# Kernel tuning notes

Hardware: AMD Instinct MI355X
Metric: run time of the kernel (lower is better)

Reference implementation:

```python
import jax, jax.numpy as jnp
import numpy as np

NCA_HIDDEN = 16
N_CODES = 32
EMBED_DIM = 64


def conv2d(x, w, pad, b=None):
    # x: (N, Cin, H, W), w: (Cout, Cin, kh, kw)
    y = jax.lax.conv_general_dilated(
        x, w, window_strides=(1, 1), padding=[(pad, pad), (pad, pad)],
        dimension_numbers=('NCHW', 'OIHW', 'NCHW'))
    if b is not None:
        y = y + b[None, :, None, None]
    return y


def setup_inputs() -> dict:
    key = jax.random.key(0)
    ks = jax.random.split(key, 32)
    rn = lambda k, shp, s=0.05: jax.random.normal(k, shp, dtype=jnp.float32) * s
    H = NCA_HIDDEN
    upd = H * H * 3 * 3  # 2304
    tau = H * H          # 256
    inp = {
        'demo_inputs':  jax.random.normal(ks[0], (8, 1, 64, 64), dtype=jnp.float32),
        'demo_outputs': jax.random.normal(ks[1], (8, 1, 64, 64), dtype=jnp.float32),
        'test_input':   jax.random.normal(ks[2], (16, 1, 256, 256), dtype=jnp.float32),
        # TaskEncoder params
        'enc_w1': rn(ks[3], (16, 2, 3, 3)),  'enc_b1': jnp.zeros((16,), jnp.float32),
        'enc_w2': rn(ks[4], (32, 16, 3, 3)), 'enc_b2': jnp.zeros((32,), jnp.float32),
        'enc_lw': rn(ks[5], (EMBED_DIM, 32)), 'enc_lb': jnp.zeros((EMBED_DIM,), jnp.float32),
        # gen_update hypernet
        'gu_w1': rn(ks[6], (128, EMBED_DIM)), 'gu_b1': jnp.zeros((128,), jnp.float32),
        'gu_w2': rn(ks[7], (upd, 128)),       'gu_b2': jnp.zeros((upd,), jnp.float32),
        # gen_tau hypernet
        'gt_w1': rn(ks[8], (64, EMBED_DIM)),  'gt_b1': jnp.zeros((64,), jnp.float32),
        'gt_w2': rn(ks[9], (tau, 64)),        'gt_b2': jnp.zeros((tau,), jnp.float32),
        # stem
        'stem_w': rn(ks[10], (H, 1, 3, 3)), 'stem_b': jnp.zeros((H,), jnp.float32),
        # VQ codebook, init U(-1/n_codes, 1/n_codes)
        'codebook': jax.random.uniform(ks[11], (N_CODES, H), jnp.float32,
                                       minval=-1.0 / N_CODES, maxval=1.0 / N_CODES),
        # decoder 1x1 conv
        'dec_w': rn(ks[12], (1, H, 1, 1)), 'dec_b': jnp.zeros((1,), jnp.float32),
        'n_steps': 5,
    }
    return inp


def reference(demo_inputs, demo_outputs, test_input,
              enc_w1, enc_b1, enc_w2, enc_b2, enc_lw, enc_lb,
              gu_w1, gu_b1, gu_w2, gu_b2,
              gt_w1, gt_b1, gt_w2, gt_b2,
              stem_w, stem_b, codebook, dec_w, dec_b, n_steps):
    H = NCA_HIDDEN
    # --- Task encoder: mean task embedding over demo pairs ---
    pairs = jnp.concatenate([demo_inputs, demo_outputs], axis=1)  # (N,2,h,w)
    h = jax.nn.relu(conv2d(pairs, enc_w1, 1, enc_b1))
    h = jax.nn.relu(conv2d(h, enc_w2, 1, enc_b2))
    h = h.mean(axis=(2, 3))                   # AdaptiveAvgPool2d(1)+Flatten -> (N,32)
    te = (h @ enc_lw.T + enc_lb).mean(axis=0)  # (embed_dim,)
    # --- Hypernetworks generate NCA weights ---
    W_update = (jax.nn.relu(te @ gu_w1.T + gu_b1) @ gu_w2.T + gu_b2).reshape(H, H, 3, 3)
    W_tau = (jax.nn.relu(te @ gt_w1.T + gt_b1) @ gt_w2.T + gt_b2).reshape(H, H, 1, 1)
    # --- Stem ---
    state = jax.nn.relu(conv2d(test_input, stem_w, 1, stem_b))  # (B,16,Hh,Ww)
    cb_sq = (codebook ** 2).sum(axis=1)  # (n_codes,)
    for _ in range(int(n_steps)):
        delta = jax.nn.relu(conv2d(state, W_update, 1))
        beta = jax.nn.sigmoid(conv2d(state, W_tau, 0))
        state = beta * state + (1.0 - beta) * delta
        # --- VQ step (straight-through) ---
        B, C, Hh, Ww = state.shape
        zf = state.transpose(0, 2, 3, 1).reshape(-1, C)  # (B*Hh*Ww, C)
        dists = (zf ** 2).sum(1, keepdims=True) + cb_sq - 2.0 * (zf @ codebook.T)
        idx = jnp.argmin(dists, axis=1)
        zq = codebook[idx].reshape(B, Hh, Ww, C).transpose(0, 3, 1, 2)
        state = state + jax.lax.stop_gradient(zq - state)
    output = jax.nn.sigmoid(conv2d(state, dec_w, 0, dec_b))
    return output
```

## Files before the change

### kernel.cpp

```cpp
#include <hip/hip_runtime.h>
#include <stdint.h>

#define NPIX 65536
#define NIMG 16

typedef float4 F4;
typedef _Float16 h2v __attribute__((ext_vector_type(2)));
typedef _Float16 h8v __attribute__((ext_vector_type(8)));
typedef float    f4v __attribute__((ext_vector_type(4)));

union H8 { h8v v; h2v p[4]; _Float16 e[8]; };

__device__ __forceinline__ float sigm(float x){ return 1.0f/(1.0f+__expf(-x)); }

#if defined(__has_builtin)
#if __has_builtin(__builtin_amdgcn_rcpf)
#define FRCP(x) __builtin_amdgcn_rcpf(x)
#endif
#endif
#ifndef FRCP
#define FRCP(x) (1.0f/(x))
#endif
__device__ __forceinline__ float sigmf(float x){ return FRCP(1.0f + __expf(-x)); }

__device__ __forceinline__ h2v pkrtz(float a, float b){
  return __builtin_bit_cast(h2v, __builtin_amdgcn_cvt_pkrtz(a,b));
}

#if defined(__has_builtin)
#if __has_builtin(__builtin_amdgcn_fdot2)
#define FDOT2(a,b,c) __builtin_amdgcn_fdot2((a),(b),(c),false)
#endif
#endif
#ifndef FDOT2
#define FDOT2(a,b,c) ((c) + (float)(a)[0]*(float)(b)[0] + (float)(a)[1]*(float)(b)[1])
#endif

__global__ __launch_bounds__(256) void k_prep(
    const float* __restrict__ w2, _Float16* __restrict__ wfragE)
{
  int t=threadIdx.x;
  for(int i=t;i<5120;i+=256){
    int j=i&7, rest=i>>3, lane=rest&63, rest2=rest>>6, ks=rest2%5, b=rest2/5;
    int g=lane>>4, nn=lane&15;
    int k=32*ks+8*g+j;
    float v=0.f;
    if(k<144){
      int tap=2*ks+(g>>1), ci=8*(g&1)+j, co=b*16+nn;
      v=w2[co*144+ci*9+tap];
    }
    wfragE[i]=(_Float16)v;
  }
}

__global__ __launch_bounds__(256) void k_enc(
    const float* __restrict__ din, const float* __restrict__ dou,
    const float* __restrict__ w1, const float* __restrict__ b1,
    const float* __restrict__ b2,
    const _Float16* __restrict__ wfragE,
    float* __restrict__ pooled)
{
  __shared__ float2 in_s[400];
  __shared__ h8v st_h[324*3];
  __shared__ float red[4][32];
  __shared__ h2v stwp_s[144];
  __shared__ h2v stbp_s[8];

  const int tid=threadIdx.x;
  const int bx=blockIdx.x, by=blockIdx.y, n=blockIdx.z;
  const float* i0 = din + n*4096;
  const float* i1 = dou + n*4096;

  for(int i=tid;i<400;i+=256){
    int sy=i/20, sx=i-sy*20;
    int gy=by*16-2+sy, gx=bx*16-2+sx;
    bool ok=((unsigned)gy<64u && (unsigned)gx<64u);
    in_s[i] = ok ? make_float2(i0[gy*64+gx], i1[gy*64+gx]) : make_float2(0.f,0.f);
  }
  if(tid<144){
    int q=tid/18, r=tid-18*q;
    stwp_s[tid]=pkrtz(w1[36*q+r], w1[36*q+18+r]);
  } else if(tid<152){
    int q=tid-144;
    stbp_s[q]=pkrtz(b1[2*q], b1[2*q+1]);
  }

  const int lane=tid&63, w=tid>>6, g=lane>>4, nn=lane&15;
  h8v B0[5], B1[5];
  const h8v* wfE=(const h8v*)wfragE;
  #pragma unroll
  for(int ks=0;ks<5;ks++){ B0[ks]=wfE[ks*64+lane]; B1[ks]=wfE[(5+ks)*64+lane]; }
  float b2a=b2[nn], b2b=b2[nn+16];
  __syncthreads();

  for(int p=tid;p<324;p+=256){
    int syh=p/18, sxh=p-syh*18;
    int gy=by*16-1+syh, gx=bx*16-1+sxh;
    H8 o0,o1;
    if((unsigned)gy<64u && (unsigned)gx<64u){
      h2v a2[8];
      #pragma unroll
      for(int q=0;q<8;q++) a2[q]=stbp_s[q];
      #pragma unroll
      for(int ky=0;ky<3;ky++){
        #pragma unroll
        for(int kx=0;kx<3;kx++){
          int tp=ky*3+kx;
          float2 v=in_s[(syh+ky)*20+(sxh+kx)];
          h2v v0=pkrtz(v.x,v.x), v1=pkrtz(v.y,v.y);
          #pragma unroll
          for(int q=0;q<8;q++){
            a2[q]=stwp_s[(2*q)*9+tp]*v0 + a2[q];
            a2[q]=stwp_s[(2*q+1)*9+tp]*v1 + a2[q];
          }
        }
      }
      o0.p[0]=a2[0]; o0.p[1]=a2[1]; o0.p[2]=a2[2]; o0.p[3]=a2[3];
      o1.p[0]=a2[4]; o1.p[1]=a2[5]; o1.p[2]=a2[6]; o1.p[3]=a2[7];
      #pragma unroll
      for(int c=0;c<8;c++){
        o0.e[c]=o0.e[c]>(_Float16)0?o0.e[c]:(_Float16)0;
        o1.e[c]=o1.e[c]>(_Float16)0?o1.e[c]:(_Float16)0;
      }
    } else {
      o0.v=(h8v){0,0,0,0,0,0,0,0};
      o1.v=(h8v){0,0,0,0,0,0,0,0};
    }
    st_h[p*3]  =o0.v;
    st_h[p*3+1]=o1.v;
  }
  __syncthreads();

  f4v acc0[4], acc1[4];
  #pragma unroll
  for(int m=0;m<4;m++){ acc0[m]=(f4v){0.f,0.f,0.f,0.f}; acc1[m]=(f4v){0.f,0.f,0.f,0.f}; }
  #pragma unroll
  for(int ks=0;ks<5;ks++){
    int t=2*ks+(g>>1); if(t>8) t=8;
    int tyo=(t*11)>>5, txo=t-tyo*3;
    int sel=g&1;
    #pragma unroll
    for(int m=0;m<4;m++){
      int sy=4*w+m+tyo;
      h8v a=st_h[(sy*18+nn+txo)*3+sel];
      acc0[m]=__builtin_amdgcn_mfma_f32_16x16x32_f16(a,B0[ks],acc0[m],0,0,0);
      acc1[m]=__builtin_amdgcn_mfma_f32_16x16x32_f16(a,B1[ks],acc1[m],0,0,0);
    }
  }
  float s0=0.f, s1=0.f;
  #pragma unroll
  for(int m=0;m<4;m++)
    #pragma unroll
    for(int r=0;r<4;r++){
      s0+=fmaxf(acc0[m][r]+b2a,0.f);
      s1+=fmaxf(acc1[m][r]+b2b,0.f);
    }
  s0+=__shfl_down(s0,32,64); s0+=__shfl_down(s0,16,64);
  s1+=__shfl_down(s1,32,64); s1+=__shfl_down(s1,16,64);
  if(lane<16){ red[w][nn]=s0; red[w][nn+16]=s1; }
  __syncthreads();
  if(tid<32){
    float s=red[0][tid]+red[1][tid]+red[2][tid]+red[3][tid];
    atomicAdd(&pooled[n*32+tid], s);
  }
}

__global__ __launch_bounds__(256) void k_hyperA(
    const float* __restrict__ pooled,
    const float* __restrict__ lw, const float* __restrict__ lb,
    const float* __restrict__ guw1, const float* __restrict__ gub1,
    const float* __restrict__ gtw1, const float* __restrict__ gtb1,
    const float* __restrict__ gtw2, const float* __restrict__ gtb2,
    const float* __restrict__ cb, const float* __restrict__ decw, const float* __restrict__ decb,
    float* __restrict__ hid_g,
    _Float16* __restrict__ wfrag_g,
    _Float16* __restrict__ Mh_g,
    _Float16* __restrict__ bcb_g, _Float16* __restrict__ omb_g,
    _Float16* __restrict__ cbh_g,
    float* __restrict__ chs_g, float* __restrict__ dvals_g)
{
  __shared__ float hm[32], te_s[64], hid_s[128], hidt_s[64];
  __shared__ float wt_s[256];
  __shared__ float cb_s[512];
  int t = threadIdx.x;
  for(int i=t;i<2560;i+=256) ((unsigned int*)wfrag_g)[i]=0u;
  for(int i=t;i<2508;i+=256) ((unsigned int*)Mh_g)[i]=0u;
  if(t<32){
    float s=0.f;
    for(int n=0;n<8;n++) s += pooled[n*32+t];
    hm[t] = s * (1.0f/32768.0f);
  }
  for(int i=t;i<512;i+=256) cb_s[i]=cb[i];
  __syncthreads();
  if(t<64){
    float s=lb[t];
    for(int c=0;c<32;c++) s = fmaf(lw[t*32+c], hm[c], s);
    te_s[t]=s;
  }
  __syncthreads();
  if(t<128){
    float s=gub1[t];
    for(int j=0;j<64;j++) s = fmaf(guw1[t*64+j], te_s[j], s);
    s=fmaxf(s,0.f);
    hid_s[t]=s; hid_g[t]=s;
  } else if(t<192){
    int i=t-128;
    float s=gtb1[i];
    for(int j=0;j<64;j++) s = fmaf(gtw1[i*64+j], te_s[j], s);
    hidt_s[i]=fmaxf(s,0.f);
  }
  __syncthreads();
  {
    float s=gtb2[t];
    for(int i=0;i<64;i++) s = fmaf(gtw2[t*64+i], hidt_s[i], s);
    int co=t>>4, ci=t&15;
    wt_s[ci*16+co]=s;
  }
  __syncthreads();
  {
    int ci=t>>4, co=t&15;
    int g=ci>>3, j=ci&7, lane=(g<<4)|co;
    wfrag_g[(448+lane)*8+j]=(_Float16)wt_s[ci*16+co];
  }
  for(int o=t;o<512;o+=256){
    int k=o>>4, c=o&15;
    float T=0.f;
    for(int ci=0;ci<16;ci++) T = fmaf(wt_s[ci*16+c], cb_s[k*16+ci], T);
    float beta=sigm(T);
    bcb_g[o]=(_Float16)(beta*cb_s[o]);
    omb_g[o]=(_Float16)(1.f-beta);
    cbh_g[o]=(_Float16)cb_s[o];
  }
  if(t<32){
    float sq=0.f, d=0.f;
    for(int c=0;c<16;c++){ float v=cb_s[t*16+c]; sq=fmaf(v,v,sq); d=fmaf(decw[c],v,d); }
    chs_g[t]=0.5f*sq;
    dvals_g[t]=sigm(d+decb[0]);
  }
}

__global__ __launch_bounds__(256) void k_hyperB(
    const float* __restrict__ guw2, const float* __restrict__ gub2,
    const float* __restrict__ hid_g, const float* __restrict__ cb,
    _Float16* __restrict__ wfrag_g, _Float16* __restrict__ Mh_g)
{
  __shared__ float hid_s[128];
  __shared__ float wu_s[256];
  __shared__ float cb_s[512];
  const int t=threadIdx.x, tp=blockIdx.x;
  if(t<128) hid_s[t]=hid_g[t];
  for(int i=t;i<512;i+=256) cb_s[i]=cb[i];
  __syncthreads();
  const int ci=t>>4, co=t&15;
  const int o=co*144+ci*9+tp;
  float s=gub2[o];
  const F4* gp=(const F4*)(guw2+(size_t)o*128);
  #pragma unroll
  for(int i=0;i<32;i++){
    F4 g=gp[i];
    s=fmaf(g.x,hid_s[4*i],s); s=fmaf(g.y,hid_s[4*i+1],s);
    s=fmaf(g.z,hid_s[4*i+2],s); s=fmaf(g.w,hid_s[4*i+3],s);
  }
  wu_s[ci*16+co]=s;
  {
    int k=tp*16+ci;
    int ks=k>>5, rem=k&31, g2=rem>>3, j=rem&7, lane=(g2<<4)|co;
    wfrag_g[(ks*64+lane)*8+j]=(_Float16)s;
  }
  __syncthreads();
  for(int o2=t;o2<512;o2+=256){
    int k=o2>>4, c=o2&15;
    float m=0.f;
    for(int c2=0;c2<16;c2++) m=fmaf(wu_s[c2*16+c], cb_s[k*16+c2], m);
    Mh_g[k*152+tp*16+c]=(_Float16)m;
  }
}

#define ST_STRIDE 3
struct S1P1 { h8v st[324*ST_STRIDE]; float in[400]; };
union S1U { S1P1 p; unsigned int dt[256*20]; };

__global__ __launch_bounds__(256) void k_step1(
    const float* __restrict__ tin,
    const float* __restrict__ stw, const float* __restrict__ stb,
    const _Float16* __restrict__ wfrag,
    const _Float16* __restrict__ cbh, const float* __restrict__ chs,
    uint8_t* __restrict__ idx_out)
{
  __shared__ S1U u;
  __shared__ h8v cb8_s[64];
  __shared__ float chs_s[32];
  __shared__ h2v stwp_s[72];
  __shared__ h2v stbp_s[8];

  const int tid=threadIdx.x;
  const int bx=blockIdx.x, by=blockIdx.y, n=blockIdx.z;
  const float* in = tin + (size_t)n*NPIX;

  for(int i=tid;i<400;i+=256){
    int sy=i/20, sx=i-sy*20;
    int gy=by*16-2+sy, gx=bx*16-2+sx;
    u.p.in[i] = ((unsigned)gy<256u && (unsigned)gx<256u) ? in[gy*256+gx] : 0.0f;
  }
  if(tid<72){
    int q=tid/9, tp=tid-q*9;
    stwp_s[q*9+tp]=pkrtz(stw[(2*q)*9+tp], stw[(2*q+1)*9+tp]);
  } else if(tid<80){
    int q=tid-72;
    stbp_s[q]=pkrtz(stb[2*q], stb[2*q+1]);
  } else if(tid>=160 && tid<192) chs_s[tid-160]=chs[tid-160];
  if(tid<64) ((uint4*)cb8_s)[tid] = ((const uint4*)cbh)[tid];

  const int lane = tid & 63, w = tid >> 6;
  const int g = lane >> 4, nn = lane & 15;
  h8v Bd[5], Bt2;
  const h8v* wf = (const h8v*)wfrag;
  #pragma unroll
  for(int ks=0;ks<5;ks++) Bd[ks]=wf[ks*64+lane];
  Bt2 = wf[7*64+lane];

  __syncthreads();

  for(int p=tid;p<324;p+=256){
    int syh=p/18, sxh=p-syh*18;
    int gy=by*16-1+syh, gx=bx*16-1+sxh;
    H8 b0,b1;
    if((unsigned)gy<256u && (unsigned)gx<256u){
      h2v a2[8];
      #pragma unroll
      for(int q=0;q<8;q++) a2[q]=stbp_s[q];
      #pragma unroll
      for(int ky=0;ky<3;ky++){
        #pragma unroll
        for(int kx=0;kx<3;kx++){
          int tp=ky*3+kx;
          float v=u.p.in[(syh+ky)*20+(sxh+kx)];
          h2v vv=pkrtz(v,v);
          #pragma unroll
          for(int q=0;q<8;q++) a2[q] = stwp_s[q*9+tp]*vv + a2[q];
        }
      }
      b0.p[0]=a2[0]; b0.p[1]=a2[1]; b0.p[2]=a2[2]; b0.p[3]=a2[3];
      b1.p[0]=a2[4]; b1.p[1]=a2[5]; b1.p[2]=a2[6]; b1.p[3]=a2[7];
      #pragma unroll
      for(int c=0;c<8;c++){
        b0.e[c]=b0.e[c]>(_Float16)0?b0.e[c]:(_Float16)0;
        b1.e[c]=b1.e[c]>(_Float16)0?b1.e[c]:(_Float16)0;
      }
    } else {
      b0.v=(h8v){0,0,0,0,0,0,0,0};
      b1.v=(h8v){0,0,0,0,0,0,0,0};
    }
    u.p.st[p*ST_STRIDE]  =b0.v;
    u.p.st[p*ST_STRIDE+1]=b1.v;
  }
  __syncthreads();

  f4v accd[4], acct[4];
  #pragma unroll
  for(int m=0;m<4;m++){ accd[m]=(f4v){0.f,0.f,0.f,0.f}; acct[m]=(f4v){0.f,0.f,0.f,0.f}; }
  #pragma unroll
  for(int ks=0;ks<5;ks++){
    int t = 2*ks + (g>>1); if(t>8) t=8;
    int tyo=(t*11)>>5, txo=t-tyo*3;
    int sel = g&1;
    #pragma unroll
    for(int m=0;m<4;m++){
      int sy = 4*w+m+tyo;
      h8v a = u.p.st[(sy*18 + nn + txo)*ST_STRIDE + sel];
      accd[m]=__builtin_amdgcn_mfma_f32_16x16x32_f16(a,Bd[ks],accd[m],0,0,0);
      if(ks==2) acct[m]=__builtin_amdgcn_mfma_f32_16x16x32_f16(a,Bt2,acct[m],0,0,0);
    }
  }
  const int py=tid>>4, pxx=tid&15;
  const int cpx=((py+1)*18+pxx+1)*ST_STRIDE;
  h8v z0=u.p.st[cpx], z1=u.p.st[cpx+1];
  __syncthreads();

  #pragma unroll
  for(int m=0;m<4;m++){
    #pragma unroll
    for(int r=0;r<4;r++){
      int px=(4*w+m)*16 + g*4 + r;
      h2v pk = pkrtz(accd[m][r], acct[m][r]);
      u.dt[px*20+nn] = __builtin_bit_cast(unsigned int, pk);
    }
  }
  __syncthreads();

  const uint4* dr=(const uint4*)(u.dt+tid*20);
  uint4 q0=dr[0],q1=dr[1],q2=dr[2],q3=dr[3];
  unsigned int qq[16]={q0.x,q0.y,q0.z,q0.w,q1.x,q1.y,q1.z,q1.w,
                       q2.x,q2.y,q2.z,q2.w,q3.x,q3.y,q3.z,q3.w};
  float zn[16];
  #pragma unroll
  for(int c=0;c<16;c++){
    h2v dt2=__builtin_bit_cast(h2v, qq[c]);
    float d=(float)dt2[0]; d = d>0.f?d:0.f;
    float beta=sigmf((float)dt2[1]);
    float zv = (c<8)? (float)z0[c] : (float)z1[c-8];
    zn[c]=fmaf(beta, zv-d, d);
  }
  H8 u0,u1;
  #pragma unroll
  for(int j=0;j<4;j++){
    u0.p[j]=pkrtz(zn[2*j],zn[2*j+1]);
    u1.p[j]=pkrtz(zn[8+2*j],zn[9+2*j]);
  }
  int best=0; float bv=-3.4e38f;
  #pragma unroll
  for(int k=0;k<32;k++){
    H8 c0,c1; c0.v=cb8_s[k*2]; c1.v=cb8_s[k*2+1];
    float dot=0.f;
    #pragma unroll
    for(int j=0;j<4;j++) dot=FDOT2(u0.p[j],c0.p[j],dot);
    #pragma unroll
    for(int j=0;j<4;j++) dot=FDOT2(u1.p[j],c1.p[j],dot);
    float val=dot-chs_s[k];
    if(val>bv){bv=val;best=k;}
  }
  idx_out[(size_t)n*NPIX + (by*16+py)*256 + (bx*16+pxx)]=(uint8_t)best;
}

__global__ __launch_bounds__(256) void k_stepN(
    const uint8_t* __restrict__ idx_in,
    const uint4* __restrict__ Mh,
    const _Float16* __restrict__ bcbh, const _Float16* __restrict__ ombh,
    const _Float16* __restrict__ cbh,  const float* __restrict__ chs,
    const float* __restrict__ dvals,
    uint8_t* __restrict__ idx_out, float* __restrict__ out, int last)
{
  __shared__ int id_s[324];
  __shared__ uint4 M_s[627];
  __shared__ h8v bcb_s[64], omb_s[64], cb8_s[64];
  __shared__ float chs_s[32], dv_s[32];
  const int tid=threadIdx.x;
  const int bx=blockIdx.x, by=blockIdx.y, n=blockIdx.z;
  const uint8_t* ip = idx_in + (size_t)n*NPIX;

  for(int i=tid;i<324;i+=256){
    int sy=i/18, sx=i-sy*18;
    int gy=by*16-1+sy, gx=bx*16-1+sx;
    id_s[i] = ((unsigned)gy<256u && (unsigned)gx<256u) ? (int)ip[gy*256+gx] : 32;
  }
  for(int i=tid;i<627;i+=256) M_s[i]=Mh[i];
  if(tid<64)        ((uint4*)bcb_s)[tid]     = ((const uint4*)bcbh)[tid];
  else if(tid<128)  ((uint4*)omb_s)[tid-64]  = ((const uint4*)ombh)[tid-64];
  else if(tid<192)  ((uint4*)cb8_s)[tid-128] = ((const uint4*)cbh)[tid-128];
  else if(tid<224)  chs_s[tid-192]=chs[tid-192];
  else              dv_s[tid-224]=dvals[tid-224];
  __syncthreads();

  const int py=tid>>4, pxx=tid&15;
  int ida[9];
  #pragma unroll
  for(int dy=0;dy<3;dy++)
    #pragma unroll
    for(int dx=0;dx<3;dx++)
      ida[dy*3+dx]=id_s[(py+dy)*18+pxx+dx];

  const h8v* Mv=(const h8v*)M_s;
  h8v a0={0,0,0,0,0,0,0,0}, a1={0,0,0,0,0,0,0,0};
  #pragma unroll
  for(int t=0;t<9;t++){
    const h8v* mp=&Mv[ida[t]*19+t*2];
    a0+=mp[0]; a1+=mp[1];
  }
  int kc=ida[4];
  h8v r0,r1;
  #pragma unroll
  for(int q=0;q<8;q++){
    r0[q]=a0[q]>(_Float16)0?a0[q]:(_Float16)0;
    r1[q]=a1[q]>(_Float16)0?a1[q]:(_Float16)0;
  }
  H8 u0,u1;
  u0.v = bcb_s[kc*2]   + omb_s[kc*2]  *r0;
  u1.v = bcb_s[kc*2+1] + omb_s[kc*2+1]*r1;
  int best=0; float bv=-3.4e38f;
  #pragma unroll
  for(int k=0;k<32;k++){
    H8 c0,c1; c0.v=cb8_s[k*2]; c1.v=cb8_s[k*2+1];
    float dot=0.f;
    #pragma unroll
    for(int j=0;j<4;j++) dot=FDOT2(u0.p[j],c0.p[j],dot);
    #pragma unroll
    for(int j=0;j<4;j++) dot=FDOT2(u1.p[j],c1.p[j],dot);
    float val=dot-chs_s[k];
    if(val>bv){bv=val;best=k;}
  }
  size_t gidx=(size_t)n*NPIX + (size_t)(by*16+py)*256 + bx*16+pxx;
  if(last) out[gidx]=dv_s[best];
  else     idx_out[gidx]=(uint8_t)best;
}

extern "C" void kernel_launch(void* const* d_in, const int* in_sizes, int n_in,
                              void* d_out, int out_size, void* d_ws, size_t ws_size,
                              hipStream_t stream)
{
  const float* demo_in  = (const float*)d_in[0];
  const float* demo_out = (const float*)d_in[1];
  const float* test_in  = (const float*)d_in[2];
  const float* enc_w1 = (const float*)d_in[3];
  const float* enc_b1 = (const float*)d_in[4];
  const float* enc_w2 = (const float*)d_in[5];
  const float* enc_b2 = (const float*)d_in[6];
  const float* enc_lw = (const float*)d_in[7];
  const float* enc_lb = (const float*)d_in[8];
  const float* gu_w1 = (const float*)d_in[9];
  const float* gu_b1 = (const float*)d_in[10];
  const float* gu_w2 = (const float*)d_in[11];
  const float* gu_b2 = (const float*)d_in[12];
  const float* gt_w1 = (const float*)d_in[13];
  const float* gt_b1 = (const float*)d_in[14];
  const float* gt_w2 = (const float*)d_in[15];
  const float* gt_b2 = (const float*)d_in[16];
  const float* stem_w = (const float*)d_in[17];
  const float* stem_b = (const float*)d_in[18];
  const float* codebook = (const float*)d_in[19];
  const float* dec_w = (const float*)d_in[20];
  const float* dec_b = (const float*)d_in[21];

  float* ws = (float*)d_ws;
  float* pooled = ws;
  float* chs    = pooled + 256;
  float* dvals  = chs + 32;
  float* hid_g  = dvals + 32;
  _Float16* hbase = (_Float16*)(ws + 448);
  _Float16* wfrag  = hbase;
  _Float16* wfragE = hbase + 5120;
  _Float16* Mh     = hbase + 10240;
  _Float16* bcbh   = hbase + 15264;
  _Float16* ombh   = hbase + 15776;
  _Float16* cbh    = hbase + 16288;
  uint8_t* idxA = (uint8_t*)(hbase + 16800);
  uint8_t* idxB = idxA + (size_t)NIMG*NPIX;

  (void)hipMemsetAsync(pooled, 0, 256*sizeof(float), stream);
  k_prep<<<1,256,0,stream>>>(enc_w2, wfragE);
  k_enc<<<dim3(4,4,8),256,0,stream>>>(demo_in, demo_out, enc_w1, enc_b1, enc_b2, wfragE, pooled);
  k_hyperA<<<1,256,0,stream>>>(pooled, enc_lw, enc_lb,
                               gu_w1,gu_b1, gt_w1,gt_b1, gt_w2,gt_b2,
                               codebook, dec_w, dec_b,
                               hid_g, wfrag, Mh, bcbh, ombh, cbh, chs, dvals);
  k_hyperB<<<9,256,0,stream>>>(gu_w2, gu_b2, hid_g, codebook, wfrag, Mh);
  dim3 tgrid(16,16,NIMG);
  k_step1<<<tgrid,256,0,stream>>>(test_in, stem_w, stem_b, wfrag, cbh, chs, idxA);
  float* outp = (float*)d_out;
  k_stepN<<<tgrid,256,0,stream>>>(idxA,(const uint4*)Mh,bcbh,ombh,cbh,chs,dvals, idxB,outp,0);
  k_stepN<<<tgrid,256,0,stream>>>(idxB,(const uint4*)Mh,bcbh,ombh,cbh,chs,dvals, idxA,outp,0);
  k_stepN<<<tgrid,256,0,stream>>>(idxA,(const uint4*)Mh,bcbh,ombh,cbh,chs,dvals, idxB,outp,0);
  k_stepN<<<tgrid,256,0,stream>>>(idxB,(const uint4*)Mh,bcbh,ombh,cbh,chs,dvals, idxA,outp,1);
}
```

Measured before the change: 250.3 us.

## Compute VQ codebook distances with MFMA and cross-lane argmin

Replaces the per-thread 32-code FDOT2 distance loop in both step kernels with a 16x16x32 f16 MFMA. Each pixel's quantized state is staged in LDS and multiplied against a pre-swizzled codebook fragment built in the hypernet kernel. The argmin is then taken with xor shuffles within each 16-lane group. This moves the scalar dot-product work onto matrix cores, at the cost of an extra LDS round trip, shuffle reductions, a wave barrier, and half of the MFMA K dimension padded with zeros.

```diff
diff --git a/kernel.cpp b/kernel.cpp
--- a/kernel.cpp
+++ b/kernel.cpp
@@ -27,14 +27,37 @@
   return __builtin_bit_cast(h2v, __builtin_amdgcn_cvt_pkrtz(a,b));
 }
 
-#if defined(__has_builtin)
-#if __has_builtin(__builtin_amdgcn_fdot2)
-#define FDOT2(a,b,c) __builtin_amdgcn_fdot2((a),(b),(c),false)
-#endif
-#endif
-#ifndef FDOT2
-#define FDOT2(a,b,c) ((c) + (float)(a)[0]*(float)(b)[0] + (float)(a)[1]*(float)(b)[1])
-#endif
+__device__ __forceinline__ int vq_mfma(
+    const _Float16* zn_s, uint8_t* bs,
+    h8v B0, h8v B1, float ch0, float ch1, int tid)
+{
+  const int lane=tid&63, wv=tid>>6, g=lane>>4, nn=lane&15;
+  __builtin_amdgcn_wave_barrier();
+  #pragma unroll
+  for(int g2=0;g2<4;g2++){
+    f4v D0={0.f,0.f,0.f,0.f}, D1={0.f,0.f,0.f,0.f};
+    h8v a=(h8v){0,0,0,0,0,0,0,0};
+    if(g<2) a=*(const h8v*)(zn_s + (wv*64+g2*16+nn)*24 + g*8);
+    D0=__builtin_amdgcn_mfma_f32_16x16x32_f16(a,B0,D0,0,0,0);
+    D1=__builtin_amdgcn_mfma_f32_16x16x32_f16(a,B1,D1,0,0,0);
+    #pragma unroll
+    for(int r=0;r<4;r++){
+      float v0=D0[r]-ch0, v1=D1[r]-ch1;
+      bool t1=v1>v0;
+      float val=t1?v1:v0; int idx=t1?nn+16:nn;
+      #pragma unroll
+      for(int mm=1;mm<16;mm<<=1){
+        float vo=__shfl_xor(val,mm,64);
+        int io=__shfl_xor(idx,mm,64);
+        bool tk=(vo>val)||((vo==val)&&(io<idx));
+        val=tk?vo:val; idx=tk?io:idx;
+      }
+      if(nn==4*g+r) bs[wv*64+g2*16+4*g+r]=(uint8_t)idx;
+    }
+  }
+  __builtin_amdgcn_wave_barrier();
+  return (int)bs[tid];
+}
 
 __global__ __launch_bounds__(256) void k_prep(
     const float* __restrict__ w2, _Float16* __restrict__ wfragE)
@@ -176,7 +199,7 @@
     _Float16* __restrict__ wfrag_g,
     _Float16* __restrict__ Mh_g,
     _Float16* __restrict__ bcb_g, _Float16* __restrict__ omb_g,
-    _Float16* __restrict__ cbh_g,
+    _Float16* __restrict__ vqb_g,
     float* __restrict__ chs_g, float* __restrict__ dvals_g)
 {
   __shared__ float hm[32], te_s[64], hid_s[128], hidt_s[64];
@@ -222,6 +245,12 @@
     int g=ci>>3, j=ci&7, lane=(g<<4)|co;
     wfrag_g[(448+lane)*8+j]=(_Float16)wt_s[ci*16+co];
   }
+  for(int i=t;i<1024;i+=256){
+    int j=i&7, lane=(i>>3)&63, b=i>>9;
+    int g=lane>>4, nn=lane&15, k=g*8+j;
+    float v=(k<16)? cb_s[(b*16+nn)*16+k] : 0.f;
+    vqb_g[i]=(_Float16)v;
+  }
   for(int o=t;o<512;o+=256){
     int k=o>>4, c=o&15;
     float T=0.f;
@@ -229,7 +258,6 @@
     float beta=sigm(T);
     bcb_g[o]=(_Float16)(beta*cb_s[o]);
     omb_g[o]=(_Float16)(1.f-beta);
-    cbh_g[o]=(_Float16)cb_s[o];
   }
   if(t<32){
     float sq=0.f, d=0.f;
@@ -278,18 +306,17 @@
 
 #define ST_STRIDE 3
 struct S1P1 { h8v st[324*ST_STRIDE]; float in[400]; };
-union S1U { S1P1 p; unsigned int dt[256*20]; };
+struct S1VQ { alignas(16) _Float16 zn[256*24]; uint8_t bs[256]; };
+union S1U { S1P1 p; unsigned int dt[256*20]; S1VQ v; };
 
 __global__ __launch_bounds__(256) void k_step1(
     const float* __restrict__ tin,
     const float* __restrict__ stw, const float* __restrict__ stb,
     const _Float16* __restrict__ wfrag,
-    const _Float16* __restrict__ cbh, const float* __restrict__ chs,
+    const _Float16* __restrict__ vqb, const float* __restrict__ chs,
     uint8_t* __restrict__ idx_out)
 {
   __shared__ S1U u;
-  __shared__ h8v cb8_s[64];
-  __shared__ float chs_s[32];
   __shared__ h2v stwp_s[72];
   __shared__ h2v stbp_s[8];
 
@@ -308,8 +335,7 @@
   } else if(tid<80){
     int q=tid-72;
     stbp_s[q]=pkrtz(stb[2*q], stb[2*q+1]);
-  } else if(tid>=160 && tid<192) chs_s[tid-160]=chs[tid-160];
-  if(tid<64) ((uint4*)cb8_s)[tid] = ((const uint4*)cbh)[tid];
+  }
 
   const int lane = tid & 63, w = tid >> 6;
   const int g = lane >> 4, nn = lane & 15;
@@ -318,6 +344,8 @@
   #pragma unroll
   for(int ks=0;ks<5;ks++) Bd[ks]=wf[ks*64+lane];
   Bt2 = wf[7*64+lane];
+  h8v VB0=((const h8v*)vqb)[lane], VB1=((const h8v*)vqb)[64+lane];
+  float ch0=chs[nn], ch1=chs[nn+16];
 
   __syncthreads();
 
@@ -407,18 +435,10 @@
     u0.p[j]=pkrtz(zn[2*j],zn[2*j+1]);
     u1.p[j]=pkrtz(zn[8+2*j],zn[9+2*j]);
   }
-  int best=0; float bv=-3.4e38f;
-  #pragma unroll
-  for(int k=0;k<32;k++){
-    H8 c0,c1; c0.v=cb8_s[k*2]; c1.v=cb8_s[k*2+1];
-    float dot=0.f;
-    #pragma unroll
-    for(int j=0;j<4;j++) dot=FDOT2(u0.p[j],c0.p[j],dot);
-    #pragma unroll
-    for(int j=0;j<4;j++) dot=FDOT2(u1.p[j],c1.p[j],dot);
-    float val=dot-chs_s[k];
-    if(val>bv){bv=val;best=k;}
-  }
+  __syncthreads();
+  *(h8v*)(u.v.zn + tid*24)     = u0.v;
+  *(h8v*)(u.v.zn + tid*24 + 8) = u1.v;
+  int best = vq_mfma(u.v.zn, u.v.bs, VB0, VB1, ch0, ch1, tid);
   idx_out[(size_t)n*NPIX + (by*16+py)*256 + (bx*16+pxx)]=(uint8_t)best;
 }
 
@@ -426,14 +446,16 @@
     const uint8_t* __restrict__ idx_in,
     const uint4* __restrict__ Mh,
     const _Float16* __restrict__ bcbh, const _Float16* __restrict__ ombh,
-    const _Float16* __restrict__ cbh,  const float* __restrict__ chs,
+    const _Float16* __restrict__ vqb,  const float* __restrict__ chs,
     const float* __restrict__ dvals,
     uint8_t* __restrict__ idx_out, float* __restrict__ out, int last)
 {
   __shared__ int id_s[324];
   __shared__ uint4 M_s[627];
-  __shared__ h8v bcb_s[64], omb_s[64], cb8_s[64];
-  __shared__ float chs_s[32], dv_s[32];
+  __shared__ h8v bcb_s[64], omb_s[64];
+  __shared__ float dv_s[32];
+  __shared__ alignas(16) _Float16 zn_s[256*24];
+  __shared__ uint8_t bs_s[256];
   const int tid=threadIdx.x;
   const int bx=blockIdx.x, by=blockIdx.y, n=blockIdx.z;
   const uint8_t* ip = idx_in + (size_t)n*NPIX;
@@ -446,9 +468,11 @@
   for(int i=tid;i<627;i+=256) M_s[i]=Mh[i];
   if(tid<64)        ((uint4*)bcb_s)[tid]     = ((const uint4*)bcbh)[tid];
   else if(tid<128)  ((uint4*)omb_s)[tid-64]  = ((const uint4*)ombh)[tid-64];
-  else if(tid<192)  ((uint4*)cb8_s)[tid-128] = ((const uint4*)cbh)[tid-128];
-  else if(tid<224)  chs_s[tid-192]=chs[tid-192];
-  else              dv_s[tid-224]=dvals[tid-224];
+  else if(tid<160)  dv_s[tid-128]=dvals[tid-128];
+
+  const int lane=tid&63, nn=lane&15;
+  h8v VB0=((const h8v*)vqb)[lane], VB1=((const h8v*)vqb)[64+lane];
+  float ch0=chs[nn], ch1=chs[nn+16];
   __syncthreads();
 
   const int py=tid>>4, pxx=tid&15;
@@ -473,21 +497,12 @@
     r0[q]=a0[q]>(_Float16)0?a0[q]:(_Float16)0;
     r1[q]=a1[q]>(_Float16)0?a1[q]:(_Float16)0;
   }
-  H8 u0,u1;
-  u0.v = bcb_s[kc*2]   + omb_s[kc*2]  *r0;
-  u1.v = bcb_s[kc*2+1] + omb_s[kc*2+1]*r1;
-  int best=0; float bv=-3.4e38f;
-  #pragma unroll
-  for(int k=0;k<32;k++){
-    H8 c0,c1; c0.v=cb8_s[k*2]; c1.v=cb8_s[k*2+1];
-    float dot=0.f;
-    #pragma unroll
-    for(int j=0;j<4;j++) dot=FDOT2(u0.p[j],c0.p[j],dot);
-    #pragma unroll
-    for(int j=0;j<4;j++) dot=FDOT2(u1.p[j],c1.p[j],dot);
-    float val=dot-chs_s[k];
-    if(val>bv){bv=val;best=k;}
-  }
+  h8v zn0 = bcb_s[kc*2]   + omb_s[kc*2]  *r0;
+  h8v zn1 = bcb_s[kc*2+1] + omb_s[kc*2+1]*r1;
+  *(h8v*)(zn_s + tid*24)     = zn0;
+  *(h8v*)(zn_s + tid*24 + 8) = zn1;
+  int best = vq_mfma(zn_s, bs_s, VB0, VB1, ch0, ch1, tid);
+
   size_t gidx=(size_t)n*NPIX + (size_t)(by*16+py)*256 + bx*16+pxx;
   if(last) out[gidx]=dv_s[best];
   else     idx_out[gidx]=(uint8_t)best;
@@ -531,8 +546,8 @@
   _Float16* Mh     = hbase + 10240;
   _Float16* bcbh   = hbase + 15264;
   _Float16* ombh   = hbase + 15776;
-  _Float16* cbh    = hbase + 16288;
-  uint8_t* idxA = (uint8_t*)(hbase + 16800);
+  _Float16* vqb    = hbase + 16288;
+  uint8_t* idxA = (uint8_t*)(hbase + 17312);
   uint8_t* idxB = idxA + (size_t)NIMG*NPIX;
 
   (void)hipMemsetAsync(pooled, 0, 256*sizeof(float), stream);
@@ -541,13 +556,13 @@
   k_hyperA<<<1,256,0,stream>>>(pooled, enc_lw, enc_lb,
                                gu_w1,gu_b1, gt_w1,gt_b1, gt_w2,gt_b2,
                                codebook, dec_w, dec_b,
-                               hid_g, wfrag, Mh, bcbh, ombh, cbh, chs, dvals);
+                               hid_g, wfrag, Mh, bcbh, ombh, vqb, chs, dvals);
   k_hyperB<<<9,256,0,stream>>>(gu_w2, gu_b2, hid_g, codebook, wfrag, Mh);
   dim3 tgrid(16,16,NIMG);
-  k_step1<<<tgrid,256,0,stream>>>(test_in, stem_w, stem_b, wfrag, cbh, chs, idxA);
+  k_step1<<<tgrid,256,0,stream>>>(test_in, stem_w, stem_b, wfrag, vqb, chs, idxA);
   float* outp = (float*)d_out;
-  k_stepN<<<tgrid,256,0,stream>>>(idxA,(const uint4*)Mh,bcbh,ombh,cbh,chs,dvals, idxB,outp,0);
-  k_stepN<<<tgrid,256,0,stream>>>(idxB,(const uint4*)Mh,bcbh,ombh,cbh,chs,dvals, idxA,outp,0);
-  k_stepN<<<tgrid,256,0,stream>>>(idxA,(const uint4*)Mh,bcbh,ombh,cbh,chs,dvals, idxB,outp,0);
-  k_stepN<<<tgrid,256,0,stream>>>(idxB,(const uint4*)Mh,bcbh,ombh,cbh,chs,dvals, idxA,outp,1);
-}
+  k_stepN<<<tgrid,256,0,stream>>>(idxA,(const uint4*)Mh,bcbh,ombh,vqb,chs,dvals, idxB,outp,0);
+  k_stepN<<<tgrid,256,0,stream>>>(idxB,(const uint4*)Mh,bcbh,ombh,vqb,chs,dvals, idxA,outp,0);
+  k_stepN<<<tgrid,256,0,stream>>>(idxA,(const uint4*)Mh,bcbh,ombh,vqb,chs,dvals, idxB,outp,0);
+  k_stepN<<<tgrid,256,0,stream>>>(idxB,(const uint4*)Mh,bcbh,ombh,vqb,chs,dvals, idxA,outp,1);
+}
```

Result: slower. 323.4 us (+29.2%).

## Fuse two NCA steps per kernel via halo recompute and merge hypernet kernels

Applied to the files above, without the earlier changes.

Each step kernel now loads a 2-pixel halo of code indices, computes the intermediate step for an 18x18 region into shared memory, and then computes the next step for the 16x16 tile. This halves the number of step launches and the global index round-trips, at the cost of recomputing about 27% extra halo pixels and adding a barrier. The two hypernet kernels are merged into a single 10-block launch that redundantly recomputes the first layer per block, and it zeroes only the padding entries instead of the whole buffer.

```diff
diff --git a/kernel.cpp b/kernel.cpp
--- a/kernel.cpp
+++ b/kernel.cpp
@@ -35,6 +35,49 @@
 #ifndef FDOT2
 #define FDOT2(a,b,c) ((c) + (float)(a)[0]*(float)(b)[0] + (float)(a)[1]*(float)(b)[1])
 #endif
+
+__device__ __forceinline__ int step_px(
+    const int* __restrict__ ids, int stride, int base,
+    const h8v* __restrict__ Mv,
+    const h8v* __restrict__ bcb_s, const h8v* __restrict__ omb_s,
+    const h8v* __restrict__ cb8_s, const float* __restrict__ chs_s)
+{
+  h8v a0={0,0,0,0,0,0,0,0}, a1={0,0,0,0,0,0,0,0};
+  int kc=0;
+  #pragma unroll
+  for(int dy=0;dy<3;dy++){
+    #pragma unroll
+    for(int dx=0;dx<3;dx++){
+      int t=dy*3+dx;
+      int kk=ids[base+dy*stride+dx];
+      if(t==4) kc=kk;
+      const h8v* mp=&Mv[kk*19+t*2];
+      a0+=mp[0]; a1+=mp[1];
+    }
+  }
+  h8v r0,r1;
+  #pragma unroll
+  for(int q=0;q<8;q++){
+    r0[q]=a0[q]>(_Float16)0?a0[q]:(_Float16)0;
+    r1[q]=a1[q]>(_Float16)0?a1[q]:(_Float16)0;
+  }
+  H8 u0,u1;
+  u0.v = bcb_s[kc*2]   + omb_s[kc*2]  *r0;
+  u1.v = bcb_s[kc*2+1] + omb_s[kc*2+1]*r1;
+  int best=0; float bv=-3.4e38f;
+  #pragma unroll
+  for(int k=0;k<32;k++){
+    H8 c0,c1; c0.v=cb8_s[k*2]; c1.v=cb8_s[k*2+1];
+    float dot=0.f;
+    #pragma unroll
+    for(int j=0;j<4;j++) dot=FDOT2(u0.p[j],c0.p[j],dot);
+    #pragma unroll
+    for(int j=0;j<4;j++) dot=FDOT2(u1.p[j],c1.p[j],dot);
+    float val=dot-chs_s[k];
+    if(val>bv){bv=val;best=k;}
+  }
+  return best;
+}
 
 __global__ __launch_bounds__(256) void k_prep(
     const float* __restrict__ w2, _Float16* __restrict__ wfragE)
@@ -165,32 +208,40 @@
   }
 }
 
-__global__ __launch_bounds__(256) void k_hyperA(
+__global__ __launch_bounds__(256) void k_hyper(
     const float* __restrict__ pooled,
     const float* __restrict__ lw, const float* __restrict__ lb,
     const float* __restrict__ guw1, const float* __restrict__ gub1,
     const float* __restrict__ gtw1, const float* __restrict__ gtb1,
     const float* __restrict__ gtw2, const float* __restrict__ gtb2,
+    const float* __restrict__ guw2, const float* __restrict__ gub2,
     const float* __restrict__ cb, const float* __restrict__ decw, const float* __restrict__ decb,
-    float* __restrict__ hid_g,
     _Float16* __restrict__ wfrag_g,
     _Float16* __restrict__ Mh_g,
     _Float16* __restrict__ bcb_g, _Float16* __restrict__ omb_g,
     _Float16* __restrict__ cbh_g,
     float* __restrict__ chs_g, float* __restrict__ dvals_g)
 {
-  __shared__ float hm[32], te_s[64], hid_s[128], hidt_s[64];
-  __shared__ float wt_s[256];
+  __shared__ float hm[32], te_s[64], hx_s[128];
+  __shared__ float wz_s[256];
   __shared__ float cb_s[512];
-  int t = threadIdx.x;
-  for(int i=t;i<2560;i+=256) ((unsigned int*)wfrag_g)[i]=0u;
-  for(int i=t;i<2508;i+=256) ((unsigned int*)Mh_g)[i]=0u;
+  const int t=threadIdx.x, blk=blockIdx.x;
   if(t<32){
     float s=0.f;
     for(int n=0;n<8;n++) s += pooled[n*32+t];
     hm[t] = s * (1.0f/32768.0f);
   }
   for(int i=t;i<512;i+=256) cb_s[i]=cb[i];
+  if(blk==9){
+    for(int i=t;i<5120;i+=256){
+      int j=i&7, rest=i>>3, lane=rest&63, rest2=rest>>6, ks=rest2%5, b=rest2/5;
+      int k=32*ks+8*(lane>>4)+j;
+      bool pad = (b==0) ? (k>=144) : ((k>>4)!=4);
+      if(pad) wfrag_g[i]=(_Float16)0.f;
+    }
+    for(int i=t;i<264;i+=256){ int k=i>>3, q=i&7; Mh_g[k*152+144+q]=(_Float16)0.f; }
+    for(int i=t;i<144;i+=256) Mh_g[32*152+i]=(_Float16)0.f;
+  }
   __syncthreads();
   if(t<64){
     float s=lb[t];
@@ -198,81 +249,70 @@
     te_s[t]=s;
   }
   __syncthreads();
-  if(t<128){
-    float s=gub1[t];
-    for(int j=0;j<64;j++) s = fmaf(guw1[t*64+j], te_s[j], s);
-    s=fmaxf(s,0.f);
-    hid_s[t]=s; hid_g[t]=s;
-  } else if(t<192){
-    int i=t-128;
-    float s=gtb1[i];
-    for(int j=0;j<64;j++) s = fmaf(gtw1[i*64+j], te_s[j], s);
-    hidt_s[i]=fmaxf(s,0.f);
-  }
-  __syncthreads();
-  {
-    float s=gtb2[t];
-    for(int i=0;i<64;i++) s = fmaf(gtw2[t*64+i], hidt_s[i], s);
-    int co=t>>4, ci=t&15;
-    wt_s[ci*16+co]=s;
-  }
-  __syncthreads();
-  {
-    int ci=t>>4, co=t&15;
-    int g=ci>>3, j=ci&7, lane=(g<<4)|co;
-    wfrag_g[(448+lane)*8+j]=(_Float16)wt_s[ci*16+co];
-  }
-  for(int o=t;o<512;o+=256){
-    int k=o>>4, c=o&15;
-    float T=0.f;
-    for(int ci=0;ci<16;ci++) T = fmaf(wt_s[ci*16+c], cb_s[k*16+ci], T);
-    float beta=sigm(T);
-    bcb_g[o]=(_Float16)(beta*cb_s[o]);
-    omb_g[o]=(_Float16)(1.f-beta);
-    cbh_g[o]=(_Float16)cb_s[o];
-  }
-  if(t<32){
-    float sq=0.f, d=0.f;
-    for(int c=0;c<16;c++){ float v=cb_s[t*16+c]; sq=fmaf(v,v,sq); d=fmaf(decw[c],v,d); }
-    chs_g[t]=0.5f*sq;
-    dvals_g[t]=sigm(d+decb[0]);
-  }
-}
-
-__global__ __launch_bounds__(256) void k_hyperB(
-    const float* __restrict__ guw2, const float* __restrict__ gub2,
-    const float* __restrict__ hid_g, const float* __restrict__ cb,
-    _Float16* __restrict__ wfrag_g, _Float16* __restrict__ Mh_g)
-{
-  __shared__ float hid_s[128];
-  __shared__ float wu_s[256];
-  __shared__ float cb_s[512];
-  const int t=threadIdx.x, tp=blockIdx.x;
-  if(t<128) hid_s[t]=hid_g[t];
-  for(int i=t;i<512;i+=256) cb_s[i]=cb[i];
-  __syncthreads();
-  const int ci=t>>4, co=t&15;
-  const int o=co*144+ci*9+tp;
-  float s=gub2[o];
-  const F4* gp=(const F4*)(guw2+(size_t)o*128);
-  #pragma unroll
-  for(int i=0;i<32;i++){
-    F4 g=gp[i];
-    s=fmaf(g.x,hid_s[4*i],s); s=fmaf(g.y,hid_s[4*i+1],s);
-    s=fmaf(g.z,hid_s[4*i+2],s); s=fmaf(g.w,hid_s[4*i+3],s);
-  }
-  wu_s[ci*16+co]=s;
-  {
-    int k=tp*16+ci;
-    int ks=k>>5, rem=k&31, g2=rem>>3, j=rem&7, lane=(g2<<4)|co;
-    wfrag_g[(ks*64+lane)*8+j]=(_Float16)s;
-  }
-  __syncthreads();
-  for(int o2=t;o2<512;o2+=256){
-    int k=o2>>4, c=o2&15;
-    float m=0.f;
-    for(int c2=0;c2<16;c2++) m=fmaf(wu_s[c2*16+c], cb_s[k*16+c2], m);
-    Mh_g[k*152+tp*16+c]=(_Float16)m;
+  if(blk<9){
+    if(t<128){
+      float s=gub1[t];
+      for(int j=0;j<64;j++) s = fmaf(guw1[t*64+j], te_s[j], s);
+      hx_s[t]=fmaxf(s,0.f);
+    }
+    __syncthreads();
+    const int ci=t>>4, co=t&15, tp=blk;
+    const int o=co*144+ci*9+tp;
+    float s=gub2[o];
+    const F4* gp=(const F4*)(guw2+(size_t)o*128);
+    #pragma unroll
+    for(int i=0;i<32;i++){
+      F4 g=gp[i];
+      s=fmaf(g.x,hx_s[4*i],s); s=fmaf(g.y,hx_s[4*i+1],s);
+      s=fmaf(g.z,hx_s[4*i+2],s); s=fmaf(g.w,hx_s[4*i+3],s);
+    }
+    wz_s[ci*16+co]=s;
+    {
+      int k=tp*16+ci;
+      int ks=k>>5, rem=k&31, g2=rem>>3, j=rem&7, lane=(g2<<4)|co;
+      wfrag_g[(ks*64+lane)*8+j]=(_Float16)s;
+    }
+    __syncthreads();
+    for(int o2=t;o2<512;o2+=256){
+      int k=o2>>4, c=o2&15;
+      float m=0.f;
+      for(int c2=0;c2<16;c2++) m=fmaf(wz_s[c2*16+c], cb_s[k*16+c2], m);
+      Mh_g[k*152+tp*16+c]=(_Float16)m;
+    }
+  } else {
+    if(t<64){
+      float s=gtb1[t];
+      for(int j=0;j<64;j++) s = fmaf(gtw1[t*64+j], te_s[j], s);
+      hx_s[t]=fmaxf(s,0.f);
+    }
+    __syncthreads();
+    {
+      float s=gtb2[t];
+      for(int i=0;i<64;i++) s = fmaf(gtw2[t*64+i], hx_s[i], s);
+      int co=t>>4, ci=t&15;
+      wz_s[ci*16+co]=s;
+    }
+    __syncthreads();
+    {
+      int ci=t>>4, co=t&15;
+      int g=ci>>3, j=ci&7, lane=(g<<4)|co;
+      wfrag_g[(448+lane)*8+j]=(_Float16)wz_s[ci*16+co];
+    }
+    for(int o=t;o<512;o+=256){
+      int k=o>>4, c=o&15;
+      float T=0.f;
+      for(int ci=0;ci<16;ci++) T = fmaf(wz_s[ci*16+c], cb_s[k*16+ci], T);
+      float beta=sigm(T);
+      bcb_g[o]=(_Float16)(beta*cb_s[o]);
+      omb_g[o]=(_Float16)(1.f-beta);
+      cbh_g[o]=(_Float16)cb_s[o];
+    }
+    if(t<32){
+      float sq=0.f, d=0.f;
+      for(int c=0;c<16;c++){ float v=cb_s[t*16+c]; sq=fmaf(v,v,sq); d=fmaf(decw[c],v,d); }
+      chs_g[t]=0.5f*sq;
+      dvals_g[t]=sigm(d+decb[0]);
+    }
   }
 }
 
@@ -422,7 +462,7 @@
   idx_out[(size_t)n*NPIX + (by*16+py)*256 + (bx*16+pxx)]=(uint8_t)best;
 }
 
-__global__ __launch_bounds__(256) void k_stepN(
+__global__ __launch_bounds__(256) void k_step2(
     const uint8_t* __restrict__ idx_in,
     const uint4* __restrict__ Mh,
     const _Float16* __restrict__ bcbh, const _Float16* __restrict__ ombh,
@@ -430,7 +470,8 @@
     const float* __restrict__ dvals,
     uint8_t* __restrict__ idx_out, float* __restrict__ out, int last)
 {
-  __shared__ int id_s[324];
+  __shared__ int idA[400];
+  __shared__ int idB[324];
   __shared__ uint4 M_s[627];
   __shared__ h8v bcb_s[64], omb_s[64], cb8_s[64];
   __shared__ float chs_s[32], dv_s[32];
@@ -438,10 +479,10 @@
   const int bx=blockIdx.x, by=blockIdx.y, n=blockIdx.z;
   const uint8_t* ip = idx_in + (size_t)n*NPIX;
 
-  for(int i=tid;i<324;i+=256){
-    int sy=i/18, sx=i-sy*18;
-    int gy=by*16-1+sy, gx=bx*16-1+sx;
-    id_s[i] = ((unsigned)gy<256u && (unsigned)gx<256u) ? (int)ip[gy*256+gx] : 32;
+  for(int i=tid;i<400;i+=256){
+    int sy=i/20, sx=i-sy*20;
+    int gy=by*16-2+sy, gx=bx*16-2+sx;
+    idA[i] = ((unsigned)gy<256u && (unsigned)gx<256u) ? (int)ip[gy*256+gx] : 32;
   }
   for(int i=tid;i<627;i+=256) M_s[i]=Mh[i];
   if(tid<64)        ((uint4*)bcb_s)[tid]     = ((const uint4*)bcbh)[tid];
@@ -451,43 +492,20 @@
   else              dv_s[tid-224]=dvals[tid-224];
   __syncthreads();
 
+  const h8v* Mv=(const h8v*)M_s;
+
+  for(int p=tid;p<324;p+=256){
+    int sy=p/18, sx=p-sy*18;
+    int gy=by*16-1+sy, gx=bx*16-1+sx;
+    int v=32;
+    if((unsigned)gy<256u && (unsigned)gx<256u)
+      v=step_px(idA,20,sy*20+sx,Mv,bcb_s,omb_s,cb8_s,chs_s);
+    idB[p]=v;
+  }
+  __syncthreads();
+
   const int py=tid>>4, pxx=tid&15;
-  int ida[9];
-  #pragma unroll
-  for(int dy=0;dy<3;dy++)
-    #pragma unroll
-    for(int dx=0;dx<3;dx++)
-      ida[dy*3+dx]=id_s[(py+dy)*18+pxx+dx];
-
-  const h8v* Mv=(const h8v*)M_s;
-  h8v a0={0,0,0,0,0,0,0,0}, a1={0,0,0,0,0,0,0,0};
-  #pragma unroll
-  for(int t=0;t<9;t++){
-    const h8v* mp=&Mv[ida[t]*19+t*2];
-    a0+=mp[0]; a1+=mp[1];
-  }
-  int kc=ida[4];
-  h8v r0,r1;
-  #pragma unroll
-  for(int q=0;q<8;q++){
-    r0[q]=a0[q]>(_Float16)0?a0[q]:(_Float16)0;
-    r1[q]=a1[q]>(_Float16)0?a1[q]:(_Float16)0;
-  }
-  H8 u0,u1;
-  u0.v = bcb_s[kc*2]   + omb_s[kc*2]  *r0;
-  u1.v = bcb_s[kc*2+1] + omb_s[kc*2+1]*r1;
-  int best=0; float bv=-3.4e38f;
-  #pragma unroll
-  for(int k=0;k<32;k++){
-    H8 c0,c1; c0.v=cb8_s[k*2]; c1.v=cb8_s[k*2+1];
-    float dot=0.f;
-    #pragma unroll
-    for(int j=0;j<4;j++) dot=FDOT2(u0.p[j],c0.p[j],dot);
-    #pragma unroll
-    for(int j=0;j<4;j++) dot=FDOT2(u1.p[j],c1.p[j],dot);
-    float val=dot-chs_s[k];
-    if(val>bv){bv=val;best=k;}
-  }
+  int best=step_px(idB,18,py*18+pxx,Mv,bcb_s,omb_s,cb8_s,chs_s);
   size_t gidx=(size_t)n*NPIX + (size_t)(by*16+py)*256 + bx*16+pxx;
   if(last) out[gidx]=dv_s[best];
   else     idx_out[gidx]=(uint8_t)best;
@@ -534,20 +552,18 @@
   _Float16* cbh    = hbase + 16288;
   uint8_t* idxA = (uint8_t*)(hbase + 16800);
   uint8_t* idxB = idxA + (size_t)NIMG*NPIX;
+  (void)hid_g;
 
   (void)hipMemsetAsync(pooled, 0, 256*sizeof(float), stream);
   k_prep<<<1,256,0,stream>>>(enc_w2, wfragE);
   k_enc<<<dim3(4,4,8),256,0,stream>>>(demo_in, demo_out, enc_w1, enc_b1, enc_b2, wfragE, pooled);
-  k_hyperA<<<1,256,0,stream>>>(pooled, enc_lw, enc_lb,
+  k_hyper<<<10,256,0,stream>>>(pooled, enc_lw, enc_lb,
                                gu_w1,gu_b1, gt_w1,gt_b1, gt_w2,gt_b2,
-                               codebook, dec_w, dec_b,
-                               hid_g, wfrag, Mh, bcbh, ombh, cbh, chs, dvals);
-  k_hyperB<<<9,256,0,stream>>>(gu_w2, gu_b2, hid_g, codebook, wfrag, Mh);
+                               gu_w2,gu_b2, codebook, dec_w, dec_b,
+                               wfrag, Mh, bcbh, ombh, cbh, chs, dvals);
   dim3 tgrid(16,16,NIMG);
   k_step1<<<tgrid,256,0,stream>>>(test_in, stem_w, stem_b, wfrag, cbh, chs, idxA);
   float* outp = (float*)d_out;
-  k_stepN<<<tgrid,256,0,stream>>>(idxA,(const uint4*)Mh,bcbh,ombh,cbh,chs,dvals, idxB,outp,0);
-  k_stepN<<<tgrid,256,0,stream>>>(idxB,(const uint4*)Mh,bcbh,ombh,cbh,chs,dvals, idxA,outp,0);
-  k_stepN<<<tgrid,256,0,stream>>>(idxA,(const uint4*)Mh,bcbh,ombh,cbh,chs,dvals, idxB,outp,0);
-  k_stepN<<<tgrid,256,0,stream>>>(idxB,(const uint4*)Mh,bcbh,ombh,cbh,chs,dvals, idxA,outp,1);
-}
+  k_step2<<<tgrid,256,0,stream>>>(idxA,(const uint4*)Mh,bcbh,ombh,cbh,chs,dvals, idxB,outp,0);
+  k_step2<<<tgrid,256,0,stream>>>(idxB,(const uint4*)Mh,bcbh,ombh,cbh,chs,dvals, idxA,outp,1);
+}
```

Result: slower. 401.8 us (+60.5%).
